# Optimization experiments

Hardware: AMD Instinct MI355X
Metric: run time of the kernel (lower is better)

## Reference

```python
import jax, jax.numpy as jnp
import numpy as np

# config
HIDDEN = 1024
NUM_EXPERTS = 16
TOP_K = 4
MOE_INTER = 512
NUM_SHARED = 2
SHARED_INTER = MOE_INTER * NUM_SHARED  # 1024
NORM_TOPK = True
ROUTED_SCALE = 1.0
NUM_TOKENS = 1024


def setup_inputs() -> dict:
    key = jax.random.key(0)
    ks = jax.random.split(key, 8)
    s = 0.02
    return {
        "hidden_states": jax.random.normal(ks[0], (NUM_TOKENS, HIDDEN), jnp.float32),
        # router (BailingMoEGate): weight [E, H], no bias
        "router_w": jax.random.normal(ks[1], (NUM_EXPERTS, HIDDEN), jnp.float32) * s,
        # routed experts: gate/up proj [E, H, I], down proj [E, I, H]
        "w_gate": jax.random.normal(ks[2], (NUM_EXPERTS, HIDDEN, MOE_INTER), jnp.float32) * s,
        "w_up": jax.random.normal(ks[3], (NUM_EXPERTS, HIDDEN, MOE_INTER), jnp.float32) * s,
        "w_down": jax.random.normal(ks[4], (NUM_EXPERTS, MOE_INTER, HIDDEN), jnp.float32) * s,
        # shared experts (BailingMoEMLP, merged gate_up): [H, 2*Is], [Is, H]
        "ws_gate_up": jax.random.normal(ks[5], (HIDDEN, 2 * SHARED_INTER), jnp.float32) * s,
        "ws_down": jax.random.normal(ks[6], (SHARED_INTER, HIDDEN), jnp.float32) * s,
    }


def _moe_forward(x, router_w, w_gate, w_up, w_down, ws_gate_up, ws_down):
    T = x.shape[0]
    # ---- router: logits -> softmax -> top-k (score_function='softmax', no bias)
    logits = jnp.einsum("th,eh->te", x, router_w)          # [T, E]
    probs = jax.nn.softmax(logits, axis=-1)
    topk_w, topk_idx = jax.lax.top_k(probs, TOP_K)         # [T, K]
    if NORM_TOPK:
        topk_w = topk_w / jnp.sum(topk_w, axis=-1, keepdims=True)
    topk_w = topk_w * ROUTED_SCALE
    # sparse combine weights [T, E] (zeros for non-selected experts)
    combine = jnp.zeros((T, NUM_EXPERTS), x.dtype).at[
        jnp.arange(T)[:, None], topk_idx
    ].set(topk_w.astype(x.dtype))
    # ---- routed experts: SiLU(x W_gate) * (x W_up) then W_down, weighted combine
    g = jnp.einsum("th,ehi->tei", x, w_gate)               # [T, E, I]
    u = jnp.einsum("th,ehi->tei", x, w_up)
    h = jax.nn.silu(g) * u
    routed = jnp.einsum("tei,eih,te->th", h, w_down, combine)
    # ---- shared experts (dense SwiGLU MLP)
    gu = x @ ws_gate_up                                    # [T, 2*Is]
    g_s, u_s = jnp.split(gu, 2, axis=-1)
    shared = (jax.nn.silu(g_s) * u_s) @ ws_down
    return routed + shared


def reference(hidden_states, router_w, w_gate, w_up, w_down, ws_gate_up, ws_down):
    return _moe_forward(hidden_states, router_w, w_gate, w_up, w_down,
                        ws_gate_up, ws_down)
```

## Files before the change

### kernel.cpp

```cpp
#include <hip/hip_runtime.h>
#include <stdint.h>


typedef __attribute__((ext_vector_type(8))) unsigned short ushort8;
typedef __attribute__((ext_vector_type(4))) float f32x4;
typedef __attribute__((ext_vector_type(8))) __bf16 bf16x8;

#define T_TOK 1024
#define HID   1024
#define NEXP  16
#define TOPK  4
#define MINTER 512
#define SINTER 1024

constexpr size_t WGU_E = 32 * 1024 * 32;
constexpr size_t WD_E  = 16 * 1024 * 32;

constexpr size_t OFF_COUNTS = 0;
constexpr size_t OFF_LIST   = 1024;
constexpr size_t OFF_WT     = OFF_LIST  + 65536;
constexpr size_t OFF_TIDX   = OFF_WT    + 65536;
constexpr size_t OFF_XB     = OFF_TIDX  + 65536;
constexpr size_t OFF_HR     = OFF_XB    + 2097152;
constexpr size_t OFF_HS     = OFF_HR    + 4194304;
constexpr size_t OFF_WGU    = OFF_HS    + 2097152;
constexpr size_t OFF_WD     = OFF_WGU   + 33554432;
constexpr size_t OFF_WSGU   = OFF_WD    + 16777216;
constexpr size_t OFF_WSD    = OFF_WSGU  + 4194304;
constexpr size_t OFF_ROUT   = OFF_WGU;

__device__ __forceinline__ unsigned short f2bf(float f) {
  union { float f; uint32_t u; } v; v.f = f;
  uint32_t r = (v.u + 0x7FFFu + ((v.u >> 16) & 1u)) >> 16;
  return (unsigned short)r;
}
__device__ __forceinline__ float bfu2f(uint32_t u) {
  union { uint32_t u; float f; } v; v.u = u << 16; return v.f;
}
__device__ __forceinline__ bf16x8 as_bf16x8(ushort8 s) {
  union { ushort8 s; bf16x8 b; } u; u.s = s; return u.b;
}
__device__ __forceinline__ float silu(float g) { return g / (1.f + __expf(-g)); }

__device__ __forceinline__ void glds16(const unsigned short* g, unsigned short* l) {
  __builtin_amdgcn_global_load_lds(
      (const __attribute__((address_space(1))) unsigned int*)g,
      (__attribute__((address_space(3))) unsigned int*)l, 16, 0, 0);
}

__global__ void init_kernel(int* counts) {
  if (threadIdx.x < NEXP) counts[threadIdx.x] = 0;
}

__global__ __launch_bounds__(64) void router_kernel(
    const float* __restrict__ x, const float* __restrict__ rw,
    int* counts, int* list, float* wt, int* tIdx,
    unsigned short* __restrict__ Xb) {
  const int t = blockIdx.x, l = threadIdx.x;
  float xv[16];
#pragma unroll
  for (int j = 0; j < 16; j++) xv[j] = x[t * HID + j * 64 + l];
#pragma unroll
  for (int j = 0; j < 16; j++) Xb[t * HID + j * 64 + l] = f2bf(xv[j]);
  float p[NEXP];
#pragma unroll
  for (int e = 0; e < NEXP; e++) {
    float s = 0.f;
#pragma unroll
    for (int j = 0; j < 16; j++) s += xv[j] * rw[e * HID + j * 64 + l];
#pragma unroll
    for (int off = 32; off > 0; off >>= 1) s += __shfl_xor(s, off);
    p[e] = s;
  }
  float mx = p[0];
#pragma unroll
  for (int e = 1; e < NEXP; e++) mx = fmaxf(mx, p[e]);
  int idx[TOPK]; float w4[TOPK]; float wsum = 0.f; unsigned used = 0u;
#pragma unroll
  for (int k = 0; k < TOPK; k++) {
    float bv = -1e30f; int bi = 0;
#pragma unroll
    for (int e = 0; e < NEXP; e++)
      if (!((used >> e) & 1u) && p[e] > bv) { bv = p[e]; bi = e; }
    used |= 1u << bi;
    idx[k] = bi;
    w4[k] = __expf(p[bi] - mx);
    wsum += w4[k];
  }
  const float inv = 1.f / wsum;
  if (l < TOPK) {
    const int e = idx[l];
    const int pos = atomicAdd(&counts[e], 1);
    list[e * 1024 + pos] = t;
    wt[e * 1024 + pos]   = w4[l] * inv;
    tIdx[t * TOPK + l]   = (e << 10) | pos;
  }
}

__global__ __launch_bounds__(256) void pack_all_kernel(
    const float* __restrict__ Wg, const float* __restrict__ Wu,
    const float* __restrict__ Wd, const float* __restrict__ Wsgu,
    const float* __restrict__ Wsd,
    unsigned short* __restrict__ WGUp, unsigned short* __restrict__ WDp,
    unsigned short* __restrict__ WSGUp, unsigned short* __restrict__ WSDp) {
  const int bid = blockIdx.x;
  const float* src; unsigned short* dst; int C, Nj, kp0, j0, r0, c0;
  if (bid < 2048) {
    const int e = bid >> 7, loc = bid & 127, kt = loc >> 3, nt = loc & 7;
    src = Wg + (size_t)e * HID * MINTER; dst = WGUp + (size_t)e * WGU_E;
    C = MINTER; Nj = 1024; kp0 = 2 * kt; j0 = nt * 128; r0 = 64 * kt; c0 = 64 * nt;
  } else if (bid < 4096) {
    const int e = (bid - 2048) >> 7, loc = bid & 127, kt = loc >> 3, nt = loc & 7;
    src = Wu + (size_t)e * HID * MINTER; dst = WGUp + (size_t)e * WGU_E;
    C = MINTER; Nj = 1024; kp0 = 2 * kt; j0 = nt * 128 + 64; r0 = 64 * kt; c0 = 64 * nt;
  } else if (bid < 6144) {
    const int e = (bid - 4096) >> 7, loc = bid & 127, kt = loc >> 4, nt = loc & 15;
    src = Wd + (size_t)e * MINTER * HID; dst = WDp + (size_t)e * WD_E;
    C = HID; Nj = 1024; kp0 = 2 * kt; j0 = 64 * nt; r0 = 64 * kt; c0 = 64 * nt;
  } else if (bid < 6656) {
    const int loc = bid - 6144, kt = loc >> 5, nt = loc & 31;
    src = Wsgu; dst = WSGUp;
    C = 2048; Nj = 2048; kp0 = 2 * kt; r0 = 64 * kt; c0 = 64 * nt;
    j0 = (nt < 16) ? nt * 128 : (nt - 16) * 128 + 64;
  } else {
    const int loc = bid - 6656, kt = loc >> 4, nt = loc & 15;
    src = Wsd; dst = WSDp;
    C = HID; Nj = 1024; kp0 = 2 * kt; j0 = 64 * nt; r0 = 64 * kt; c0 = 64 * nt;
  }
  __shared__ float tile[64][65];
  const int t = threadIdx.x;
  {
    const int r = t >> 4, c4 = (t & 15) * 4;
#pragma unroll
    for (int p = 0; p < 4; p++) {
      const int rr = p * 16 + r;
      const float4 v = *(const float4*)(src + (size_t)(r0 + rr) * C + c0 + c4);
      tile[rr][c4 + 0] = v.x; tile[rr][c4 + 1] = v.y;
      tile[rr][c4 + 2] = v.z; tile[rr][c4 + 3] = v.w;
    }
  }
  __syncthreads();
  {
    const int n = t >> 2, k8 = (t & 3) * 8;
#pragma unroll
    for (int h = 0; h < 2; h++) {
      const int k = 32 * h + k8;
      union { unsigned short u[8]; ushort8 v; } pk;
#pragma unroll
      for (int i = 0; i < 8; i++) pk.u[i] = f2bf(tile[k + i][n]);
      *(ushort8*)(dst + ((size_t)(kp0 + h) * Nj + j0 + n) * 32 + k8) = pk.v;
    }
  }
}

__global__ __launch_bounds__(256, 4) void phase1_kernel(
    const unsigned short* __restrict__ Xb,
    const unsigned short* __restrict__ WGUp,
    const unsigned short* __restrict__ WSGUp,
    const int* __restrict__ counts, const int* __restrict__ list,
    const float* __restrict__ wt,
    unsigned short* __restrict__ Hr,
    unsigned short* __restrict__ Hs) {
  const int z = blockIdx.z, x = blockIdx.x, y = blockIdx.y;
  const bool routed = (z < NEXP);
  int cnt = 0, base = 0;
  if (routed) {
    if (x >= 8) return;
    cnt = counts[z];
    if (y * 64 >= cnt) return;
#pragma unroll
    for (int i = 0; i < NEXP; i++) base += (i < z) ? counts[i] : 0;
  }
  __shared__ __align__(16) unsigned short sA[64 * 32];
  __shared__ __align__(16) unsigned short sB[128 * 32];
  const int tid = threadIdx.x, w = tid >> 6, l = tid & 63;
  const int m0 = y * 64;
  const int swz = ((l & 3) ^ ((l >> 3) & 3)) * 8;
  const size_t NjStep = (size_t)(routed ? 1024 : 2048) * 32;

  const unsigned short* aS;
  {
    const int r = m0 + 16 * w + (l >> 2);
    const unsigned short* row = routed
        ? Xb + (size_t)list[z * 1024 + min(r, cnt - 1)] * HID
        : Xb + (size_t)r * HID;
    aS = row + swz;
  }
  const unsigned short* pan = routed ? WGUp + (size_t)z * WGU_E : WSGUp;
  const unsigned short* bS[2];
#pragma unroll
  for (int ii = 0; ii < 2; ii++) {
    const int j = x * 128 + 32 * w + 16 * ii + (l >> 2);
    bS[ii] = pan + (size_t)j * 32 + swz;
  }
  const int rsw = ((l >> 4) ^ (((l & 15) >> 1) & 3)) * 8;
  const int aOff = (16 * w + (l & 15)) * 32 + rsw;
  int bOff[8];
#pragma unroll
  for (int jt = 0; jt < 8; jt++) bOff[jt] = (16 * jt + (l & 15)) * 32 + rsw;

  f32x4 acc[8];
#pragma unroll
  for (int jt = 0; jt < 8; jt++) acc[jt] = (f32x4){0.f, 0.f, 0.f, 0.f};

#pragma unroll 1
  for (int s = 0; s < HID / 32; s++) {
    __syncthreads();
    glds16(aS + s * 32, sA + (16 * w) * 32);
    glds16(bS[0] + s * NjStep, sB + (32 * w) * 32);
    glds16(bS[1] + s * NjStep, sB + (32 * w + 16) * 32);
    __syncthreads();
    const bf16x8 af = as_bf16x8(*(const ushort8*)(sA + aOff));
#pragma unroll
    for (int jt = 0; jt < 8; jt++) {
      const bf16x8 bf = as_bf16x8(*(const ushort8*)(sB + bOff[jt]));
      acc[jt] = __builtin_amdgcn_mfma_f32_16x16x32_bf16(af, bf, acc[jt], 0, 0, 0);
    }
  }

  const int rl = (l >> 4) * 4;
#pragma unroll
  for (int jt = 0; jt < 4; jt++) {
    const int c = 64 * x + 16 * jt + (l & 15);
#pragma unroll
    for (int r = 0; r < 4; r++) {
      const int grow = m0 + 16 * w + rl + r;
      const float g = acc[jt][r], u = acc[jt + 4][r];
      if (routed) {
        if (grow < cnt) {
          const float h = silu(g) * u * wt[z * 1024 + grow];
          Hr[((size_t)(c >> 5) * 4096 + base + grow) * 32 + (c & 31)] = f2bf(h);
        }
      } else {
        const float h = silu(g) * u;
        Hs[((size_t)(c >> 5) * 1024 + grow) * 32 + (c & 31)] = f2bf(h);
      }
    }
  }
}

__global__ __launch_bounds__(256, 4) void phase2_kernel(
    const unsigned short* __restrict__ Hr, const unsigned short* __restrict__ Hs,
    const unsigned short* __restrict__ WDp, const unsigned short* __restrict__ WSDp,
    const int* __restrict__ counts,
    unsigned short* __restrict__ Rout,
    float* __restrict__ out) {
  const int z = blockIdx.z, x = blockIdx.x, y = blockIdx.y;
  const bool routed = (z < NEXP);
  int cnt = 0, base = 0, steps;
  if (routed) {
    cnt = counts[z];
    if (y * 64 >= cnt) return;
#pragma unroll
    for (int i = 0; i < NEXP; i++) base += (i < z) ? counts[i] : 0;
    steps = MINTER / 32;
  } else {
    steps = SINTER / 32;
  }
  __shared__ __align__(16) unsigned short sA[64 * 32];
  __shared__ __align__(16) unsigned short sB[128 * 32];
  const int tid = threadIdx.x, w = tid >> 6, l = tid & 63;
  const int m0 = y * 64;
  const int swz = ((l & 3) ^ ((l >> 3) & 3)) * 8;
  const size_t strideA = (size_t)(routed ? 4096 : 1024) * 32;
  const size_t strideB = (size_t)1024 * 32;

  const unsigned short* aS;
  {
    const int r = 16 * w + (l >> 2);
    const int R = routed ? (base + min(m0 + r, cnt - 1)) : (m0 + r);
    aS = (routed ? Hr : Hs) + (size_t)R * 32 + swz;
  }
  const unsigned short* pan = routed ? WDp + (size_t)z * WD_E : WSDp;
  const unsigned short* bS[2];
#pragma unroll
  for (int ii = 0; ii < 2; ii++) {
    const int j = x * 128 + 32 * w + 16 * ii + (l >> 2);
    bS[ii] = pan + (size_t)j * 32 + swz;
  }
  const int rsw = ((l >> 4) ^ (((l & 15) >> 1) & 3)) * 8;
  const int aOff = (16 * w + (l & 15)) * 32 + rsw;
  int bOff[8];
#pragma unroll
  for (int jt = 0; jt < 8; jt++) bOff[jt] = (16 * jt + (l & 15)) * 32 + rsw;

  f32x4 acc[8];
#pragma unroll
  for (int jt = 0; jt < 8; jt++) acc[jt] = (f32x4){0.f, 0.f, 0.f, 0.f};

#pragma unroll 1
  for (int s = 0; s < steps; s++) {
    __syncthreads();
    glds16(aS + s * strideA, sA + (16 * w) * 32);
    glds16(bS[0] + s * strideB, sB + (32 * w) * 32);
    glds16(bS[1] + s * strideB, sB + (32 * w + 16) * 32);
    __syncthreads();
    const bf16x8 af = as_bf16x8(*(const ushort8*)(sA + aOff));
#pragma unroll
    for (int jt = 0; jt < 8; jt++) {
      const bf16x8 bf = as_bf16x8(*(const ushort8*)(sB + bOff[jt]));
      acc[jt] = __builtin_amdgcn_mfma_f32_16x16x32_bf16(af, bf, acc[jt], 0, 0, 0);
    }
  }

  const int rl = (l >> 4) * 4;
#pragma unroll
  for (int jt = 0; jt < 8; jt++) {
    const int col = 128 * x + 16 * jt + (l & 15);
#pragma unroll
    for (int r = 0; r < 4; r++) {
      const int grow = m0 + 16 * w + rl + r;
      if (routed) {
        if (grow < cnt)
          Rout[(size_t)(base + grow) * HID + col] = f2bf(acc[jt][r]);
      } else {
        out[(size_t)grow * HID + col] = acc[jt][r];
      }
    }
  }
}

__global__ __launch_bounds__(256) void combine_kernel(
    const unsigned short* __restrict__ Rout, const int* __restrict__ counts,
    const int* __restrict__ tIdx, float* __restrict__ out) {
  __shared__ int sb[NEXP];
  if (threadIdx.x == 0) {
    int s = 0;
#pragma unroll
    for (int e = 0; e < NEXP; e++) { sb[e] = s; s += counts[e]; }
  }
  __syncthreads();
  const int t = blockIdx.x, c4 = threadIdx.x * 4;
  float4 o = *(const float4*)(out + (size_t)t * HID + c4);
#pragma unroll
  for (int k = 0; k < TOPK; k++) {
    const int v = tIdx[t * TOPK + k];
    const int row = sb[v >> 10] + (v & 1023);
    const uint2 rv = *(const uint2*)(Rout + (size_t)row * HID + c4);
    o.x += bfu2f(rv.x & 0xffffu); o.y += bfu2f(rv.x >> 16);
    o.z += bfu2f(rv.y & 0xffffu); o.w += bfu2f(rv.y >> 16);
  }
  *(float4*)(out + (size_t)t * HID + c4) = o;
}

extern "C" void kernel_launch(void* const* d_in, const int* in_sizes, int n_in,
                              void* d_out, int out_size, void* d_ws, size_t ws_size,
                              hipStream_t stream) {
  const float* x      = (const float*)d_in[0];
  const float* rw     = (const float*)d_in[1];
  const float* w_gate = (const float*)d_in[2];
  const float* w_up   = (const float*)d_in[3];
  const float* w_down = (const float*)d_in[4];
  const float* ws_gu  = (const float*)d_in[5];
  const float* ws_dn  = (const float*)d_in[6];
  float* out = (float*)d_out;
  char* ws = (char*)d_ws;

  int*   counts = (int*)  (ws + OFF_COUNTS);
  int*   list   = (int*)  (ws + OFF_LIST);
  float* wtbuf  = (float*)(ws + OFF_WT);
  int*   tIdx   = (int*)  (ws + OFF_TIDX);
  unsigned short* Xb    = (unsigned short*)(ws + OFF_XB);
  unsigned short* Hr    = (unsigned short*)(ws + OFF_HR);
  unsigned short* Hs    = (unsigned short*)(ws + OFF_HS);
  unsigned short* WGUp  = (unsigned short*)(ws + OFF_WGU);
  unsigned short* WDp   = (unsigned short*)(ws + OFF_WD);
  unsigned short* WSGUp = (unsigned short*)(ws + OFF_WSGU);
  unsigned short* WSDp  = (unsigned short*)(ws + OFF_WSD);
  unsigned short* Rout  = (unsigned short*)(ws + OFF_ROUT);

  init_kernel<<<1, 64, 0, stream>>>(counts);
  router_kernel<<<T_TOK, 64, 0, stream>>>(x, rw, counts, list, wtbuf, tIdx, Xb);
  pack_all_kernel<<<6912, 256, 0, stream>>>(
      w_gate, w_up, w_down, ws_gu, ws_dn, WGUp, WDp, WSGUp, WSDp);
  phase1_kernel<<<dim3(16, 16, 17), 256, 0, stream>>>(
      Xb, WGUp, WSGUp, counts, list, wtbuf, Hr, Hs);
  phase2_kernel<<<dim3(8, 16, 17), 256, 0, stream>>>(
      Hr, Hs, WDp, WSDp, counts, Rout, out);
  combine_kernel<<<T_TOK, 256, 0, stream>>>(Rout, counts, tIdx, out);
  (void)in_sizes; (void)n_in; (void)out_size; (void)ws_size;
}
```

Measured before the change: 246.4 us.

## Triple-buffer LDS loads and retile MoE GEMMs to 128x64 warp grid

Both expert GEMM kernels now use a three-stage LDS ring buffer. Loads for step s+2 are issued while step s computes, and a partial vmcnt wait replaces the two __syncthreads per step. The block tile changes from 64x128 to 128x64 with a 2x2 warp layout of 64x32 per warp, which raises A-fragment reuse across MFMAs. The weight packing interleaves gate and up columns in 16-wide groups so each block's 64-column slice holds matching gate/up pairs. The cost is more LDS per block (about 36KB), which can lower occupancy, and coarser row tiles that waste more work on small expert counts.

```diff
diff --git a/kernel.cpp b/kernel.cpp
--- a/kernel.cpp
+++ b/kernel.cpp
@@ -48,6 +48,9 @@
       (__attribute__((address_space(3))) unsigned int*)l, 16, 0, 0);
 }
 
+#define PIPE_BARRIER3() asm volatile("s_waitcnt vmcnt(3) lgkmcnt(0)\ns_barrier" ::: "memory")
+#define PIPE_BARRIER0() asm volatile("s_waitcnt vmcnt(0) lgkmcnt(0)\ns_barrier" ::: "memory")
+
 __global__ void init_kernel(int* counts) {
   if (threadIdx.x < NEXP) counts[threadIdx.x] = 0;
 }
@@ -104,28 +107,33 @@
     unsigned short* __restrict__ WGUp, unsigned short* __restrict__ WDp,
     unsigned short* __restrict__ WSGUp, unsigned short* __restrict__ WSDp) {
   const int bid = blockIdx.x;
-  const float* src; unsigned short* dst; int C, Nj, kp0, j0, r0, c0;
+  const float* src; unsigned short* dst; int C, Nj, kp0, r0, c0, jbase, ilv;
   if (bid < 2048) {
     const int e = bid >> 7, loc = bid & 127, kt = loc >> 3, nt = loc & 7;
     src = Wg + (size_t)e * HID * MINTER; dst = WGUp + (size_t)e * WGU_E;
-    C = MINTER; Nj = 1024; kp0 = 2 * kt; j0 = nt * 128; r0 = 64 * kt; c0 = 64 * nt;
+    C = MINTER; Nj = 1024; kp0 = 2 * kt; r0 = 64 * kt; c0 = 64 * nt;
+    jbase = 128 * nt; ilv = 1;
   } else if (bid < 4096) {
     const int e = (bid - 2048) >> 7, loc = bid & 127, kt = loc >> 3, nt = loc & 7;
     src = Wu + (size_t)e * HID * MINTER; dst = WGUp + (size_t)e * WGU_E;
-    C = MINTER; Nj = 1024; kp0 = 2 * kt; j0 = nt * 128 + 64; r0 = 64 * kt; c0 = 64 * nt;
+    C = MINTER; Nj = 1024; kp0 = 2 * kt; r0 = 64 * kt; c0 = 64 * nt;
+    jbase = 128 * nt + 16; ilv = 1;
   } else if (bid < 6144) {
     const int e = (bid - 4096) >> 7, loc = bid & 127, kt = loc >> 4, nt = loc & 15;
     src = Wd + (size_t)e * MINTER * HID; dst = WDp + (size_t)e * WD_E;
-    C = HID; Nj = 1024; kp0 = 2 * kt; j0 = 64 * nt; r0 = 64 * kt; c0 = 64 * nt;
+    C = HID; Nj = 1024; kp0 = 2 * kt; r0 = 64 * kt; c0 = 64 * nt;
+    jbase = 64 * nt; ilv = 0;
   } else if (bid < 6656) {
     const int loc = bid - 6144, kt = loc >> 5, nt = loc & 31;
     src = Wsgu; dst = WSGUp;
     C = 2048; Nj = 2048; kp0 = 2 * kt; r0 = 64 * kt; c0 = 64 * nt;
-    j0 = (nt < 16) ? nt * 128 : (nt - 16) * 128 + 64;
+    const int isU = (nt >= 16), ntc = nt & 15;
+    jbase = 128 * ntc + 16 * isU; ilv = 1;
   } else {
     const int loc = bid - 6656, kt = loc >> 4, nt = loc & 15;
     src = Wsd; dst = WSDp;
-    C = HID; Nj = 1024; kp0 = 2 * kt; j0 = 64 * nt; r0 = 64 * kt; c0 = 64 * nt;
+    C = HID; Nj = 1024; kp0 = 2 * kt; r0 = 64 * kt; c0 = 64 * nt;
+    jbase = 64 * nt; ilv = 0;
   }
   __shared__ float tile[64][65];
   const int t = threadIdx.x;
@@ -142,13 +150,14 @@
   __syncthreads();
   {
     const int n = t >> 2, k8 = (t & 3) * 8;
+    const int j = jbase + (ilv ? (32 * (n >> 4) + (n & 15)) : n);
 #pragma unroll
     for (int h = 0; h < 2; h++) {
       const int k = 32 * h + k8;
       union { unsigned short u[8]; ushort8 v; } pk;
 #pragma unroll
       for (int i = 0; i < 8; i++) pk.u[i] = f2bf(tile[k + i][n]);
-      *(ushort8*)(dst + ((size_t)(kp0 + h) * Nj + j0 + n) * 32 + k8) = pk.v;
+      *(ushort8*)(dst + ((size_t)(kp0 + h) * Nj + j) * 32 + k8) = pk.v;
     }
   }
 }
@@ -165,78 +174,90 @@
   const bool routed = (z < NEXP);
   int cnt = 0, base = 0;
   if (routed) {
-    if (x >= 8) return;
+    if (x >= 16) return;
     cnt = counts[z];
-    if (y * 64 >= cnt) return;
+    if (y * 128 >= cnt) return;
 #pragma unroll
     for (int i = 0; i < NEXP; i++) base += (i < z) ? counts[i] : 0;
   }
-  __shared__ __align__(16) unsigned short sA[64 * 32];
-  __shared__ __align__(16) unsigned short sB[128 * 32];
+  __shared__ __align__(16) unsigned short sA[3][128 * 32];
+  __shared__ __align__(16) unsigned short sB[3][64 * 32];
   const int tid = threadIdx.x, w = tid >> 6, l = tid & 63;
-  const int m0 = y * 64;
+  const int wm = w >> 1, wn = w & 1, m0 = y * 128;
   const int swz = ((l & 3) ^ ((l >> 3) & 3)) * 8;
-  const size_t NjStep = (size_t)(routed ? 1024 : 2048) * 32;
-
-  const unsigned short* aS;
-  {
-    const int r = m0 + 16 * w + (l >> 2);
+  const int Nj = routed ? 1024 : 2048;
+
+  const unsigned short* aS[2];
+#pragma unroll
+  for (int ii = 0; ii < 2; ii++) {
+    const int r = 32 * w + 16 * ii + (l >> 2);
     const unsigned short* row = routed
-        ? Xb + (size_t)list[z * 1024 + min(r, cnt - 1)] * HID
-        : Xb + (size_t)r * HID;
-    aS = row + swz;
+        ? Xb + (size_t)list[z * 1024 + min(m0 + r, cnt - 1)] * HID
+        : Xb + (size_t)(m0 + r) * HID;
+    aS[ii] = row + swz;
   }
   const unsigned short* pan = routed ? WGUp + (size_t)z * WGU_E : WSGUp;
-  const unsigned short* bS[2];
-#pragma unroll
-  for (int ii = 0; ii < 2; ii++) {
-    const int j = x * 128 + 32 * w + 16 * ii + (l >> 2);
-    bS[ii] = pan + (size_t)j * 32 + swz;
-  }
+  const unsigned short* bS = pan + ((size_t)(x * 64 + 16 * w + (l >> 2))) * 32 + swz;
+  const size_t bStep = (size_t)Nj * 32;
+
   const int rsw = ((l >> 4) ^ (((l & 15) >> 1) & 3)) * 8;
-  const int aOff = (16 * w + (l & 15)) * 32 + rsw;
-  int bOff[8];
-#pragma unroll
-  for (int jt = 0; jt < 8; jt++) bOff[jt] = (16 * jt + (l & 15)) * 32 + rsw;
-
-  f32x4 acc[8];
-#pragma unroll
-  for (int jt = 0; jt < 8; jt++) acc[jt] = (f32x4){0.f, 0.f, 0.f, 0.f};
-
+  int aOff[4], bOff[2];
+#pragma unroll
+  for (int i = 0; i < 4; i++) aOff[i] = (wm * 64 + 16 * i + (l & 15)) * 32 + rsw;
+#pragma unroll
+  for (int jt = 0; jt < 2; jt++) bOff[jt] = (wn * 32 + 16 * jt + (l & 15)) * 32 + rsw;
+
+  f32x4 acc[4][2];
+#pragma unroll
+  for (int i = 0; i < 4; i++)
+#pragma unroll
+    for (int jt = 0; jt < 2; jt++) acc[i][jt] = (f32x4){0.f, 0.f, 0.f, 0.f};
+
+  auto stage = [&](int s, int b) {
+    glds16(aS[0] + s * 32, &sA[b][(32 * w) * 32]);
+    glds16(aS[1] + s * 32, &sA[b][(32 * w + 16) * 32]);
+    glds16(bS + s * bStep, &sB[b][(16 * w) * 32]);
+  };
+
+  const int steps = HID / 32;
+  stage(0, 0); stage(1, 1);
 #pragma unroll 1
-  for (int s = 0; s < HID / 32; s++) {
-    __syncthreads();
-    glds16(aS + s * 32, sA + (16 * w) * 32);
-    glds16(bS[0] + s * NjStep, sB + (32 * w) * 32);
-    glds16(bS[1] + s * NjStep, sB + (32 * w + 16) * 32);
-    __syncthreads();
-    const bf16x8 af = as_bf16x8(*(const ushort8*)(sA + aOff));
-#pragma unroll
-    for (int jt = 0; jt < 8; jt++) {
-      const bf16x8 bf = as_bf16x8(*(const ushort8*)(sB + bOff[jt]));
-      acc[jt] = __builtin_amdgcn_mfma_f32_16x16x32_bf16(af, bf, acc[jt], 0, 0, 0);
-    }
-  }
-
-  const int rl = (l >> 4) * 4;
-#pragma unroll
-  for (int jt = 0; jt < 4; jt++) {
-    const int c = 64 * x + 16 * jt + (l & 15);
+  for (int s = 0; s < steps; s++) {
+    const int cb = s % 3;
+    if (s + 2 < steps) { PIPE_BARRIER3(); stage(s + 2, (s + 2) % 3); }
+    else if (s + 1 < steps) { PIPE_BARRIER3(); }
+    else { PIPE_BARRIER0(); }
+    const unsigned short* A = &sA[cb][0];
+    const unsigned short* B = &sB[cb][0];
+    bf16x8 af[4], bfr[2];
+#pragma unroll
+    for (int i = 0; i < 4; i++) af[i] = as_bf16x8(*(const ushort8*)(A + aOff[i]));
+#pragma unroll
+    for (int jt = 0; jt < 2; jt++) bfr[jt] = as_bf16x8(*(const ushort8*)(B + bOff[jt]));
+#pragma unroll
+    for (int jt = 0; jt < 2; jt++)
+#pragma unroll
+      for (int i = 0; i < 4; i++)
+        acc[i][jt] = __builtin_amdgcn_mfma_f32_16x16x32_bf16(af[i], bfr[jt], acc[i][jt], 0, 0, 0);
+  }
+
+  const int rl = (l >> 4) * 4, pc = 16 * wn + (l & 15);
+#pragma unroll
+  for (int i = 0; i < 4; i++)
 #pragma unroll
     for (int r = 0; r < 4; r++) {
-      const int grow = m0 + 16 * w + rl + r;
-      const float g = acc[jt][r], u = acc[jt + 4][r];
+      const int grow = m0 + wm * 64 + 16 * i + rl + r;
+      const float g = acc[i][0][r], u = acc[i][1][r];
       if (routed) {
         if (grow < cnt) {
           const float h = silu(g) * u * wt[z * 1024 + grow];
-          Hr[((size_t)(c >> 5) * 4096 + base + grow) * 32 + (c & 31)] = f2bf(h);
+          Hr[((size_t)x * 4096 + base + grow) * 32 + pc] = f2bf(h);
         }
       } else {
         const float h = silu(g) * u;
-        Hs[((size_t)(c >> 5) * 1024 + grow) * 32 + (c & 31)] = f2bf(h);
+        Hs[((size_t)x * 1024 + grow) * 32 + pc] = f2bf(h);
       }
     }
-  }
 }
 
 __global__ __launch_bounds__(256, 4) void phase2_kernel(
@@ -250,74 +271,88 @@
   int cnt = 0, base = 0, steps;
   if (routed) {
     cnt = counts[z];
-    if (y * 64 >= cnt) return;
+    if (y * 128 >= cnt) return;
 #pragma unroll
     for (int i = 0; i < NEXP; i++) base += (i < z) ? counts[i] : 0;
     steps = MINTER / 32;
   } else {
     steps = SINTER / 32;
   }
-  __shared__ __align__(16) unsigned short sA[64 * 32];
-  __shared__ __align__(16) unsigned short sB[128 * 32];
+  __shared__ __align__(16) unsigned short sA[3][128 * 32];
+  __shared__ __align__(16) unsigned short sB[3][64 * 32];
   const int tid = threadIdx.x, w = tid >> 6, l = tid & 63;
-  const int m0 = y * 64;
+  const int wm = w >> 1, wn = w & 1, m0 = y * 128;
   const int swz = ((l & 3) ^ ((l >> 3) & 3)) * 8;
-  const size_t strideA = (size_t)(routed ? 4096 : 1024) * 32;
-  const size_t strideB = (size_t)1024 * 32;
-
-  const unsigned short* aS;
-  {
-    const int r = 16 * w + (l >> 2);
+  const size_t aStep = (size_t)(routed ? 4096 : 1024) * 32;
+
+  const unsigned short* aS[2];
+#pragma unroll
+  for (int ii = 0; ii < 2; ii++) {
+    const int r = 32 * w + 16 * ii + (l >> 2);
     const int R = routed ? (base + min(m0 + r, cnt - 1)) : (m0 + r);
-    aS = (routed ? Hr : Hs) + (size_t)R * 32 + swz;
+    aS[ii] = (routed ? Hr : Hs) + (size_t)R * 32 + swz;
   }
   const unsigned short* pan = routed ? WDp + (size_t)z * WD_E : WSDp;
-  const unsigned short* bS[2];
-#pragma unroll
-  for (int ii = 0; ii < 2; ii++) {
-    const int j = x * 128 + 32 * w + 16 * ii + (l >> 2);
-    bS[ii] = pan + (size_t)j * 32 + swz;
-  }
+  const unsigned short* bS = pan + ((size_t)(x * 64 + 16 * w + (l >> 2))) * 32 + swz;
+  const size_t bStep = (size_t)1024 * 32;
+
   const int rsw = ((l >> 4) ^ (((l & 15) >> 1) & 3)) * 8;
-  const int aOff = (16 * w + (l & 15)) * 32 + rsw;
-  int bOff[8];
-#pragma unroll
-  for (int jt = 0; jt < 8; jt++) bOff[jt] = (16 * jt + (l & 15)) * 32 + rsw;
-
-  f32x4 acc[8];
-#pragma unroll
-  for (int jt = 0; jt < 8; jt++) acc[jt] = (f32x4){0.f, 0.f, 0.f, 0.f};
-
+  int aOff[4], bOff[2];
+#pragma unroll
+  for (int i = 0; i < 4; i++) aOff[i] = (wm * 64 + 16 * i + (l & 15)) * 32 + rsw;
+#pragma unroll
+  for (int jt = 0; jt < 2; jt++) bOff[jt] = (wn * 32 + 16 * jt + (l & 15)) * 32 + rsw;
+
+  f32x4 acc[4][2];
+#pragma unroll
+  for (int i = 0; i < 4; i++)
+#pragma unroll
+    for (int jt = 0; jt < 2; jt++) acc[i][jt] = (f32x4){0.f, 0.f, 0.f, 0.f};
+
+  auto stage = [&](int s, int b) {
+    glds16(aS[0] + s * aStep, &sA[b][(32 * w) * 32]);
+    glds16(aS[1] + s * aStep, &sA[b][(32 * w + 16) * 32]);
+    glds16(bS + s * bStep, &sB[b][(16 * w) * 32]);
+  };
+
+  stage(0, 0); stage(1, 1);
 #pragma unroll 1
   for (int s = 0; s < steps; s++) {
-    __syncthreads();
-    glds16(aS + s * strideA, sA + (16 * w) * 32);
-    glds16(bS[0] + s * strideB, sB + (32 * w) * 32);
-    glds16(bS[1] + s * strideB, sB + (32 * w + 16) * 32);
-    __syncthreads();
-    const bf16x8 af = as_bf16x8(*(const ushort8*)(sA + aOff));
-#pragma unroll
-    for (int jt = 0; jt < 8; jt++) {
-      const bf16x8 bf = as_bf16x8(*(const ushort8*)(sB + bOff[jt]));
-      acc[jt] = __builtin_amdgcn_mfma_f32_16x16x32_bf16(af, bf, acc[jt], 0, 0, 0);
-    }
+    const int cb = s % 3;
+    if (s + 2 < steps) { PIPE_BARRIER3(); stage(s + 2, (s + 2) % 3); }
+    else if (s + 1 < steps) { PIPE_BARRIER3(); }
+    else { PIPE_BARRIER0(); }
+    const unsigned short* A = &sA[cb][0];
+    const unsigned short* B = &sB[cb][0];
+    bf16x8 af[4], bfr[2];
+#pragma unroll
+    for (int i = 0; i < 4; i++) af[i] = as_bf16x8(*(const ushort8*)(A + aOff[i]));
+#pragma unroll
+    for (int jt = 0; jt < 2; jt++) bfr[jt] = as_bf16x8(*(const ushort8*)(B + bOff[jt]));
+#pragma unroll
+    for (int jt = 0; jt < 2; jt++)
+#pragma unroll
+      for (int i = 0; i < 4; i++)
+        acc[i][jt] = __builtin_amdgcn_mfma_f32_16x16x32_bf16(af[i], bfr[jt], acc[i][jt], 0, 0, 0);
   }
 
   const int rl = (l >> 4) * 4;
 #pragma unroll
-  for (int jt = 0; jt < 8; jt++) {
-    const int col = 128 * x + 16 * jt + (l & 15);
+  for (int i = 0; i < 4; i++)
 #pragma unroll
     for (int r = 0; r < 4; r++) {
-      const int grow = m0 + 16 * w + rl + r;
-      if (routed) {
-        if (grow < cnt)
-          Rout[(size_t)(base + grow) * HID + col] = f2bf(acc[jt][r]);
-      } else {
-        out[(size_t)grow * HID + col] = acc[jt][r];
+      const int grow = m0 + wm * 64 + 16 * i + rl + r;
+#pragma unroll
+      for (int jt = 0; jt < 2; jt++) {
+        const int col = 64 * x + 32 * wn + 16 * jt + (l & 15);
+        if (routed) {
+          if (grow < cnt)
+            Rout[(size_t)(base + grow) * HID + col] = f2bf(acc[i][jt][r]);
+        } else {
+          out[(size_t)grow * HID + col] = acc[i][jt][r];
+        }
       }
     }
-  }
 }
 
 __global__ __launch_bounds__(256) void combine_kernel(
@@ -373,9 +408,9 @@
   router_kernel<<<T_TOK, 64, 0, stream>>>(x, rw, counts, list, wtbuf, tIdx, Xb);
   pack_all_kernel<<<6912, 256, 0, stream>>>(
       w_gate, w_up, w_down, ws_gu, ws_dn, WGUp, WDp, WSGUp, WSDp);
-  phase1_kernel<<<dim3(16, 16, 17), 256, 0, stream>>>(
+  phase1_kernel<<<dim3(32, 8, 17), 256, 0, stream>>>(
       Xb, WGUp, WSGUp, counts, list, wtbuf, Hr, Hs);
-  phase2_kernel<<<dim3(8, 16, 17), 256, 0, stream>>>(
+  phase2_kernel<<<dim3(16, 8, 17), 256, 0, stream>>>(
       Hr, Hs, WDp, WSDp, counts, Rout, out);
   combine_kernel<<<T_TOK, 256, 0, stream>>>(Rout, counts, tIdx, out);
   (void)in_sizes; (void)n_in; (void)out_size; (void)ws_size;
```

Measured after the change: 243.5 us. Within noise of the previous version (-1.2%).
